# Kernel tuning notes

Hardware: AMD Instinct MI355X
Metric: run time of the kernel (lower is better)

## Reference

```python
import jax, jax.numpy as jnp
import numpy as np

B, L1, L2, H = 16, 1024, 1024, 768

def setup_inputs() -> dict:
    key = jax.random.key(0)
    k1, k2, k3, k4, k5, k6 = jax.random.split(key, 6)
    x1 = jax.random.normal(k1, (B, L1, H), dtype=jnp.float32)
    x2 = jax.random.normal(k2, (B, L2, H), dtype=jnp.float32)
    # True = padded position (masked out), matching torch masked_fill_ semantics
    x1_mask = jax.random.randint(k3, (B, L1), 0, 2) == 1
    x2_mask = jax.random.randint(k4, (B, L2), 0, 2) == 1
    # shared nn.Linear(H, H) used for both x and y projections
    W = jax.random.normal(k5, (H, H), dtype=jnp.float32) / np.sqrt(H)
    b = jax.random.normal(k6, (H,), dtype=jnp.float32) * 0.01
    return {"x1": x1, "x2": x2, "x1_mask": x1_mask, "x2_mask": x2_mask, "W": W, "b": b}

def reference(x1, x2, x1_mask, x2_mask, W, b):
    # SeqAttnMatch('relu_FC', normalize='sumY') with z = y = x2
    x_proj = jax.nn.relu(jnp.einsum('bid,hd->bih', x1, W) + b)   # [B,L1,H]
    y_proj = jax.nn.relu(jnp.einsum('bjd,hd->bjh', x2, W) + b)   # [B,L2,H]
    scores = jnp.einsum('bih,bjh->bij', x_proj, y_proj)          # [B,L1,L2]
    scores = jnp.where(x2_mask[:, None, :], -jnp.inf, scores)
    alpha = jax.nn.softmax(scores, axis=-1)                      # sum over len2
    att = jnp.einsum('bij,bjd->bid', alpha, x2)                  # [B,L1,H]
    # inter_att_concat = 'concat_dot_diff'
    return jnp.concatenate([x1, att, x1 * att, x1 - att], axis=2)  # [B,L1,4H]
```

## Files before the change

### kernel.cpp

```cpp
#include <hip/hip_runtime.h>


#define B_  16
#define L_  1024
#define H_  768
#define M1_ (B_ * L_)
#define MT_ (2 * M1_)

#define XB_  24576
#define WB_  576
#define TB_  3072

using f32x4  = __attribute__((ext_vector_type(4))) float;
using bf16x8 = __attribute__((ext_vector_type(8))) __bf16;
using u16x8  = __attribute__((ext_vector_type(8))) unsigned short;
using u16x4  = __attribute__((ext_vector_type(4))) unsigned short;

__device__ inline unsigned short f2b(float f) {
  unsigned u = __builtin_bit_cast(unsigned, f);
  u += 0x7FFFu + ((u >> 16) & 1u);
  return (unsigned short)(u >> 16);
}
__device__ inline float b2f(unsigned short u) {
  return __builtin_bit_cast(float, ((unsigned)u) << 16);
}

__device__ inline void gld16(const void* g, void* l) {
  __builtin_amdgcn_global_load_lds(
      (__attribute__((address_space(1))) void*)g,
      (__attribute__((address_space(3))) void*)l, 16, 0, 0);
}

__device__ inline bf16x8 ld_frag_sw(const unsigned short* lds, int row, int quad) {
  const int sl = quad ^ ((row >> 1) & 3);
  u16x8 v = *(const u16x8*)(lds + row * 32 + sl * 8);
  return __builtin_bit_cast(bf16x8, v);
}

#define MFMA(a, b, c) __builtin_amdgcn_mfma_f32_16x16x32_bf16((a), (b), (c), 0, 0, 0)

__device__ __forceinline__ void stage2(const unsigned short* __restrict__ src,
                                       unsigned short* ldsbase,
                                       int wv, int lq, int lsw,
                                       size_t row0, int k0) {
#pragma unroll
  for (int g = 0; g < 2; ++g) {
    const int rowl = wv * 32 + g * 16;
    gld16(src + (row0 + rowl + lq) * (size_t)H_ + k0 + lsw * 8,
          ldsbase + rowl * 32);
  }
}

__device__ __forceinline__ void gemm3_loop(
    const unsigned short* __restrict__ Agh, const unsigned short* __restrict__ Agl,
    const unsigned short* __restrict__ Bgh, const unsigned short* __restrict__ Bgl,
    size_t arow0, size_t brow0,
    unsigned short* SA, unsigned short* SB, f32x4 (&acc)[8][4])
{
  const int tid  = threadIdx.x;
  const int lane = tid & 63, wv = tid >> 6;
  const int wr = wv >> 2, wc = wv & 3;
  const int quad = lane >> 4, lx = lane & 15;
  const int lq  = lane >> 2;
  const int lsw = (lane & 3) ^ ((lane >> 3) & 3);
  constexpr int HB = 256 * 32;

  stage2(Agh, SA,      wv, lq, lsw, arow0, 0);
  stage2(Bgh, SB,      wv, lq, lsw, brow0, 0);
  stage2(Agl, SA + HB, wv, lq, lsw, arow0, 0);
  stage2(Bgl, SB + HB, wv, lq, lsw, brow0, 0);
  asm volatile("s_waitcnt vmcnt(4)" ::: "memory");
  __builtin_amdgcn_s_barrier();

  int c = 0;
  for (int t = 0; t < H_ / 32; ++t) {
    unsigned short* sAh = SA + c * (2 * HB);
    unsigned short* sAl = sAh + HB;
    unsigned short* sBh = SB + c * (2 * HB);
    unsigned short* sBl = sBh + HB;
    unsigned short* dA  = SA + (c ^ 1) * (2 * HB);
    unsigned short* dB  = SB + (c ^ 1) * (2 * HB);
    const int  k1   = t * 32 + 32;
    const bool more = (t < H_ / 32 - 1);

    bf16x8 fah[8], fbh[4];
#pragma unroll
    for (int i = 0; i < 8; ++i) fah[i] = ld_frag_sw(sAh, wr * 128 + i * 16 + lx, quad);
#pragma unroll
    for (int j = 0; j < 4; ++j) fbh[j] = ld_frag_sw(sBh, wc * 64 + j * 16 + lx, quad);
    if (more) {
      stage2(Agh, dA,      wv, lq, lsw, arow0, k1);
      stage2(Bgh, dB,      wv, lq, lsw, brow0, k1);
      stage2(Agl, dA + HB, wv, lq, lsw, arow0, k1);
      stage2(Bgl, dB + HB, wv, lq, lsw, brow0, k1);
    }
    __builtin_amdgcn_s_barrier();
    __builtin_amdgcn_s_setprio(1);
#pragma unroll
    for (int i = 0; i < 8; ++i)
#pragma unroll
      for (int j = 0; j < 4; ++j) acc[i][j] = MFMA(fah[i], fbh[j], acc[i][j]);
    __builtin_amdgcn_s_setprio(0);
    if (more) asm volatile("s_waitcnt vmcnt(8)" ::: "memory");
    else      asm volatile("s_waitcnt vmcnt(0)" ::: "memory");
    __builtin_amdgcn_s_barrier();

    bf16x8 fbl[4];
#pragma unroll
    for (int j = 0; j < 4; ++j) fbl[j] = ld_frag_sw(sBl, wc * 64 + j * 16 + lx, quad);
    __builtin_amdgcn_s_barrier();
    __builtin_amdgcn_s_setprio(1);
#pragma unroll
    for (int i = 0; i < 8; ++i)
#pragma unroll
      for (int j = 0; j < 4; ++j) acc[i][j] = MFMA(fah[i], fbl[j], acc[i][j]);
    __builtin_amdgcn_s_setprio(0);
    __builtin_amdgcn_s_barrier();

    bf16x8 fal[8];
#pragma unroll
    for (int i = 0; i < 8; ++i) fal[i] = ld_frag_sw(sAl, wr * 128 + i * 16 + lx, quad);
    __builtin_amdgcn_s_barrier();
    __builtin_amdgcn_s_setprio(1);
#pragma unroll
    for (int i = 0; i < 8; ++i)
#pragma unroll
      for (int j = 0; j < 4; ++j) acc[i][j] = MFMA(fal[i], fbh[j], acc[i][j]);
    __builtin_amdgcn_s_setprio(0);
    if (more) asm volatile("s_waitcnt vmcnt(4)" ::: "memory");
    __builtin_amdgcn_s_barrier();

    c ^= 1;
  }
}

__global__ __launch_bounds__(256) void k_split(
    const float* __restrict__ x1, const float* __restrict__ x2,
    const float* __restrict__ W,
    unsigned short* __restrict__ Xh, unsigned short* __restrict__ Xl,
    unsigned short* __restrict__ Wh, unsigned short* __restrict__ Wl,
    unsigned short* __restrict__ x2T)
{
  __shared__ unsigned short tile[64][72];
  const int tid = threadIdx.x;
  const int bx  = blockIdx.x;

  if (bx < XB_) {
    const size_t idx = (size_t)bx * 256 + tid;
    const int row = (int)(idx / 192);
    const int col = ((int)(idx % 192)) * 4;
    const float* src = (row < M1_) ? (x1 + (size_t)row * H_ + col)
                                   : (x2 + (size_t)(row - M1_) * H_ + col);
    f32x4 v = *(const f32x4*)src;
    u16x4 h, l;
#pragma unroll
    for (int q = 0; q < 4; ++q) { h[q] = f2b(v[q]); l[q] = f2b(v[q] - b2f(h[q])); }
    *(u16x4*)(Xh + idx * 4) = h;
    *(u16x4*)(Xl + idx * 4) = l;
  } else if (bx < XB_ + WB_) {
    const int idx = (bx - XB_) * 256 + tid;
    f32x4 v = *(const f32x4*)(W + (size_t)idx * 4);
    u16x4 h, l;
#pragma unroll
    for (int q = 0; q < 4; ++q) { h[q] = f2b(v[q]); l[q] = f2b(v[q] - b2f(h[q])); }
    *(u16x4*)(Wh + (size_t)idx * 4) = h;
    *(u16x4*)(Wl + (size_t)idx * 4) = l;
  } else {
    const int t  = bx - (XB_ + WB_);
    const int b  = t / 192;
    const int r  = t % 192;
    const int j0 = (r / 12) * 64;
    const int d0 = (r % 12) * 64;
#pragma unroll
    for (int p = 0; p < 4; ++p) {
      const int idx = tid + p * 256;
      const int jr  = idx >> 4;
      const int dc  = (idx & 15) * 4;
      f32x4 v = *(const f32x4*)(x2 + ((size_t)(b * L_ + j0 + jr)) * H_ + d0 + dc);
#pragma unroll
      for (int q = 0; q < 4; ++q) tile[jr][dc + q] = f2b(v[q]);
    }
    __syncthreads();
#pragma unroll
    for (int p = 0; p < 2; ++p) {
      const int idx = tid + p * 256;
      const int dr  = idx >> 3;
      const int jc  = (idx & 7) * 8;
      u16x8 o;
#pragma unroll
      for (int q = 0; q < 8; ++q) o[q] = tile[jc + q][dr];
      *(u16x8*)(x2T + ((size_t)(b * H_) + d0 + dr) * L_ + j0 + jc) = o;
    }
  }
}

__global__ __launch_bounds__(512, 2) void k_proj(
    const unsigned short* __restrict__ Xh, const unsigned short* __restrict__ Xl,
    const unsigned short* __restrict__ Wh, const unsigned short* __restrict__ Wl,
    const float* __restrict__ bias,
    unsigned short* __restrict__ Ph, unsigned short* __restrict__ Pl)
{
  __shared__ unsigned short SA[2 * 2 * 256 * 32];
  __shared__ unsigned short SB[2 * 2 * 256 * 32];

  const int tid  = threadIdx.x;
  const int lane = tid & 63, wv = tid >> 6;
  const int wr = wv >> 2, wc = wv & 3;
  const int quad = lane >> 4, lx = lane & 15;

  const int lin = blockIdx.x;
  const int s   = (lin & 7) * 48 + (lin >> 3);
  const int n0  = (s % 3) * 256;
  const int m0  = (s / 3) * 256;

  f32x4 acc[8][4] = {};
  gemm3_loop(Xh, Xl, Wh, Wl, (size_t)m0, (size_t)n0, SA, SB, acc);

#pragma unroll
  for (int j = 0; j < 4; ++j) {
    const int h = n0 + wc * 64 + j * 16 + lx;
    const float bv = bias[h];
#pragma unroll
    for (int i = 0; i < 8; ++i) {
      const int mrow = m0 + wr * 128 + i * 16 + quad * 4;
#pragma unroll
      for (int r = 0; r < 4; ++r) {
        float v = acc[i][j][r] + bv;
        v = v > 0.f ? v : 0.f;
        const unsigned short hh = f2b(v);
        const unsigned short ll = f2b(v - b2f(hh));
        const size_t off = (size_t)(mrow + r) * H_ + h;
        Ph[off] = hh;
        Pl[off] = ll;
      }
    }
  }
}

__global__ __launch_bounds__(512, 2) void k_scores(
    const unsigned short* __restrict__ Ph, const unsigned short* __restrict__ Pl,
    const int* __restrict__ x2_mask, float* __restrict__ scores)
{
  __shared__ unsigned short SA[2 * 2 * 256 * 32];
  __shared__ unsigned short SB[2 * 2 * 256 * 32];

  const int tid  = threadIdx.x;
  const int lane = tid & 63, wv = tid >> 6;
  const int wr = wv >> 2, wc = wv & 3;
  const int quad = lane >> 4, lx = lane & 15;

  const int lin = blockIdx.x;
  const int s   = (lin & 7) * 32 + (lin >> 3);
  const int j0  = (s & 3) * 256;
  const int i0  = ((s >> 2) & 3) * 256;
  const int b   = s >> 4;

  f32x4 acc[8][4] = {};
  gemm3_loop(Ph, Pl, Ph, Pl,
             (size_t)(b * L_ + i0), (size_t)(M1_ + b * L_ + j0), SA, SB, acc);

#pragma unroll
  for (int j = 0; j < 4; ++j) {
    const int jj = j0 + wc * 64 + j * 16 + lx;
    const int mv = x2_mask[b * L_ + jj];
#pragma unroll
    for (int i = 0; i < 8; ++i) {
      const int ib = i0 + wr * 128 + i * 16 + quad * 4;
#pragma unroll
      for (int r = 0; r < 4; ++r) {
        const float v = mv ? -1e30f : acc[i][j][r];
        scores[((size_t)(b * L_) + ib + r) * L_ + jj] = v;
      }
    }
  }
}

__global__ __launch_bounds__(256) void k_softmax(
    const float* __restrict__ scores, unsigned short* __restrict__ alphab)
{
  const size_t row = blockIdx.x;
  const float* p = scores + row * L_;
  const int tid = threadIdx.x;

  f32x4 v = *(const f32x4*)(p + tid * 4);
  float m = fmaxf(fmaxf(v[0], v[1]), fmaxf(v[2], v[3]));
#pragma unroll
  for (int off = 32; off > 0; off >>= 1) m = fmaxf(m, __shfl_down(m, off));

  __shared__ float rmax[4];
  __shared__ float rsum[4];
  const int wid = tid >> 6, lane = tid & 63;
  if (lane == 0) rmax[wid] = m;
  __syncthreads();
  m = fmaxf(fmaxf(rmax[0], rmax[1]), fmaxf(rmax[2], rmax[3]));

  f32x4 e;
#pragma unroll
  for (int q = 0; q < 4; ++q) e[q] = __expf(v[q] - m);
  float s = e[0] + e[1] + e[2] + e[3];
#pragma unroll
  for (int off = 32; off > 0; off >>= 1) s += __shfl_down(s, off);
  if (lane == 0) rsum[wid] = s;
  __syncthreads();
  s = rsum[0] + rsum[1] + rsum[2] + rsum[3];

  const float inv = 1.0f / s;
  u16x4 o;
#pragma unroll
  for (int q = 0; q < 4; ++q) o[q] = f2b(e[q] * inv);
  *(u16x4*)(alphab + row * L_ + tid * 4) = o;
}

__global__ __launch_bounds__(256) void k_att(
    const unsigned short* __restrict__ alphab, const unsigned short* __restrict__ x2T,
    float* __restrict__ att)
{
  __shared__ unsigned short Aa[128 * 32];
  __shared__ unsigned short Bt[128 * 32];

  const int tid  = threadIdx.x;
  const int lane = tid & 63, wv = tid >> 6;
  const int wr = wv >> 1, wc = wv & 1;
  const int quad = lane >> 4, lx = lane & 15;
  const int lr = lane >> 2, ls = lane & 3;
  const int lsw = ls ^ ((lr >> 1) & 3);

  const int lin = blockIdx.x;
  const int s   = (lin & 7) * 96 + (lin >> 3);
  const int d0  = (s % 6) * 128;
  const int i0  = ((s / 6) & 7) * 128;
  const int b   = s / 48;

  f32x4 acc[4][4] = {};

  for (int j0 = 0; j0 < L_; j0 += 32) {
    __syncthreads();
#pragma unroll
    for (int g = 0; g < 2; ++g) {
      const int rowl = wv * 32 + g * 16;
      const int row  = rowl + lr;
      const size_t ga = (size_t)(b * L_ + i0 + row) * L_ + j0 + lsw * 8;
      const size_t gb = ((size_t)(b * H_) + d0 + row) * L_ + j0 + lsw * 8;
      gld16(alphab + ga, &Aa[rowl * 32]);
      gld16(x2T + gb, &Bt[rowl * 32]);
    }
    __syncthreads();

    bf16x8 fa[4], fb[4];
#pragma unroll
    for (int t = 0; t < 4; ++t) {
      fa[t] = ld_frag_sw(Aa, wr * 64 + t * 16 + lx, quad);
      fb[t] = ld_frag_sw(Bt, wc * 64 + t * 16 + lx, quad);
    }
#pragma unroll
    for (int i = 0; i < 4; ++i)
#pragma unroll
      for (int j = 0; j < 4; ++j)
        acc[i][j] = MFMA(fa[i], fb[j], acc[i][j]);
  }

#pragma unroll
  for (int j = 0; j < 4; ++j) {
    const int dd = d0 + wc * 64 + j * 16 + lx;
#pragma unroll
    for (int i = 0; i < 4; ++i) {
      const int ib = i0 + wr * 64 + i * 16 + quad * 4;
#pragma unroll
      for (int r = 0; r < 4; ++r)
        att[((size_t)(b * L_) + ib + r) * H_ + dd] = acc[i][j][r];
    }
  }
}

__global__ __launch_bounds__(256) void k_concat(
    const float* __restrict__ x1, const float* __restrict__ att,
    float* __restrict__ out)
{
  const int gid = blockIdx.x * 256 + threadIdx.x;
  const int row = gid / 192;
  const int c   = (gid % 192) * 4;

  f32x4 xv = *(const f32x4*)(x1  + (size_t)row * H_ + c);
  f32x4 av = *(const f32x4*)(att + (size_t)row * H_ + c);
  f32x4 mv, sv;
#pragma unroll
  for (int q = 0; q < 4; ++q) { mv[q] = xv[q] * av[q]; sv[q] = xv[q] - av[q]; }

  float* ob = out + (size_t)row * (4 * H_) + c;
  *(f32x4*)(ob)          = xv;
  *(f32x4*)(ob + H_)     = av;
  *(f32x4*)(ob + 2 * H_) = mv;
  *(f32x4*)(ob + 3 * H_) = sv;
}

extern "C" void kernel_launch(void* const* d_in, const int* in_sizes, int n_in,
                              void* d_out, int out_size, void* d_ws, size_t ws_size,
                              hipStream_t stream) {
  const float* x1      = (const float*)d_in[0];
  const float* x2      = (const float*)d_in[1];
  const int*   x2_mask = (const int*)d_in[3];
  const float* W       = (const float*)d_in[4];
  const float* bias    = (const float*)d_in[5];
  float* out = (float*)d_out;

  char* o8 = (char*)d_out;
  unsigned short* Ph     = (unsigned short*)o8;
  unsigned short* Pl     = (unsigned short*)(o8 + 50331648);
  float*          scores = (float*)(o8 + 100663296);
  unsigned short* Xh     = (unsigned short*)(o8 + 100663296);
  unsigned short* Wh     = (unsigned short*)(o8 + 167772160);
  unsigned short* Wl     = (unsigned short*)(o8 + 168951808);
  unsigned short* x2T    = (unsigned short*)(o8 + 170131456);
  unsigned short* alphab = (unsigned short*)o8;
  unsigned short* Xl     = (unsigned short*)d_ws;
  float*          att    = (float*)d_ws;

  k_split  <<<dim3(XB_ + WB_ + TB_), 256, 0, stream>>>(x1, x2, W, Xh, Xl, Wh, Wl, x2T);
  k_proj   <<<dim3(384),   512, 0, stream>>>(Xh, Xl, Wh, Wl, bias, Ph, Pl);
  k_scores <<<dim3(256),   512, 0, stream>>>(Ph, Pl, x2_mask, scores);
  k_softmax<<<dim3(16384), 256, 0, stream>>>(scores, alphab);
  k_att    <<<dim3(768),   256, 0, stream>>>(alphab, x2T, att);
  k_concat <<<dim3(12288), 256, 0, stream>>>(x1, att, out);
}
```

Baseline: 644.0 us.

## Halve projection GEMM M-tile and stagger low-half loads across MFMA phases

The projection GEMM now uses 128x256 tiles instead of 256x256, which doubles the block count to 768 and halves the A-side shared memory. The shared GEMM loop is templated on the M-fragment count. Prefetches of the low-precision halves (Bl, Al) are moved later so they overlap the intermediate MFMA phases rather than all being issued at once, with vmcnt waits adjusted to match. This aims to improve CU occupancy and wave balance for the projection and to spread memory traffic through the loop. The cost is less operand reuse per block in the projection and more intricate wait-count bookkeeping.

```diff
diff --git a/kernel.cpp b/kernel.cpp
--- a/kernel.cpp
+++ b/kernel.cpp
@@ -39,95 +39,106 @@
 
 #define MFMA(a, b, c) __builtin_amdgcn_mfma_f32_16x16x32_bf16((a), (b), (c), 0, 0, 0)
 
-__device__ __forceinline__ void stage2(const unsigned short* __restrict__ src,
+template<int CH>
+__device__ __forceinline__ void stageH(const unsigned short* __restrict__ src,
                                        unsigned short* ldsbase,
                                        int wv, int lq, int lsw,
                                        size_t row0, int k0) {
 #pragma unroll
-  for (int g = 0; g < 2; ++g) {
-    const int rowl = wv * 32 + g * 16;
+  for (int g = 0; g < CH; ++g) {
+    const int rowl = wv * (CH * 16) + g * 16;
     gld16(src + (row0 + rowl + lq) * (size_t)H_ + k0 + lsw * 8,
           ldsbase + rowl * 32);
   }
 }
 
+template<int MI>
 __device__ __forceinline__ void gemm3_loop(
     const unsigned short* __restrict__ Agh, const unsigned short* __restrict__ Agl,
     const unsigned short* __restrict__ Bgh, const unsigned short* __restrict__ Bgl,
     size_t arow0, size_t brow0,
-    unsigned short* SA, unsigned short* SB, f32x4 (&acc)[8][4])
-{
+    unsigned short* SA, unsigned short* SB, f32x4 (&acc)[MI][4])
+{
+  constexpr int CA  = MI / 4;
+  constexpr int HBA = (MI * 32) * 32;
+  constexpr int HBB = 256 * 32;
+
   const int tid  = threadIdx.x;
   const int lane = tid & 63, wv = tid >> 6;
   const int wr = wv >> 2, wc = wv & 3;
   const int quad = lane >> 4, lx = lane & 15;
   const int lq  = lane >> 2;
   const int lsw = (lane & 3) ^ ((lane >> 3) & 3);
-  constexpr int HB = 256 * 32;
-
-  stage2(Agh, SA,      wv, lq, lsw, arow0, 0);
-  stage2(Bgh, SB,      wv, lq, lsw, brow0, 0);
-  stage2(Agl, SA + HB, wv, lq, lsw, arow0, 0);
-  stage2(Bgl, SB + HB, wv, lq, lsw, brow0, 0);
-  asm volatile("s_waitcnt vmcnt(4)" ::: "memory");
+
+  stageH<CA>(Agh, SA,       wv, lq, lsw, arow0, 0);
+  stageH<2 >(Bgh, SB,       wv, lq, lsw, brow0, 0);
+  stageH<2 >(Bgl, SB + HBB, wv, lq, lsw, brow0, 0);
+  stageH<CA>(Agl, SA + HBA, wv, lq, lsw, arow0, 0);
+  asm volatile("s_waitcnt vmcnt(%0)" :: "i"(CA + 2) : "memory");
   __builtin_amdgcn_s_barrier();
 
   int c = 0;
   for (int t = 0; t < H_ / 32; ++t) {
-    unsigned short* sAh = SA + c * (2 * HB);
-    unsigned short* sAl = sAh + HB;
-    unsigned short* sBh = SB + c * (2 * HB);
-    unsigned short* sBl = sBh + HB;
-    unsigned short* dA  = SA + (c ^ 1) * (2 * HB);
-    unsigned short* dB  = SB + (c ^ 1) * (2 * HB);
+    unsigned short* sAh = SA + c * (2 * HBA);
+    unsigned short* sAl = sAh + HBA;
+    unsigned short* sBh = SB + c * (2 * HBB);
+    unsigned short* sBl = sBh + HBB;
+    unsigned short* dA  = SA + (c ^ 1) * (2 * HBA);
+    unsigned short* dB  = SB + (c ^ 1) * (2 * HBB);
     const int  k1   = t * 32 + 32;
     const bool more = (t < H_ / 32 - 1);
 
-    bf16x8 fah[8], fbh[4];
-#pragma unroll
-    for (int i = 0; i < 8; ++i) fah[i] = ld_frag_sw(sAh, wr * 128 + i * 16 + lx, quad);
-#pragma unroll
-    for (int j = 0; j < 4; ++j) fbh[j] = ld_frag_sw(sBh, wc * 64 + j * 16 + lx, quad);
+    bf16x8 fah[MI], fbh[4];
+#pragma unroll
+    for (int i = 0; i < MI; ++i)
+      fah[i] = ld_frag_sw(sAh, wr * (MI * 16) + i * 16 + lx, quad);
+#pragma unroll
+    for (int j = 0; j < 4; ++j)
+      fbh[j] = ld_frag_sw(sBh, wc * 64 + j * 16 + lx, quad);
     if (more) {
-      stage2(Agh, dA,      wv, lq, lsw, arow0, k1);
-      stage2(Bgh, dB,      wv, lq, lsw, brow0, k1);
-      stage2(Agl, dA + HB, wv, lq, lsw, arow0, k1);
-      stage2(Bgl, dB + HB, wv, lq, lsw, brow0, k1);
+      stageH<CA>(Agh, dA, wv, lq, lsw, arow0, k1);
+      stageH<2 >(Bgh, dB, wv, lq, lsw, brow0, k1);
     }
     __builtin_amdgcn_s_barrier();
     __builtin_amdgcn_s_setprio(1);
 #pragma unroll
-    for (int i = 0; i < 8; ++i)
+    for (int i = 0; i < MI; ++i)
 #pragma unroll
       for (int j = 0; j < 4; ++j) acc[i][j] = MFMA(fah[i], fbh[j], acc[i][j]);
     __builtin_amdgcn_s_setprio(0);
-    if (more) asm volatile("s_waitcnt vmcnt(8)" ::: "memory");
-    else      asm volatile("s_waitcnt vmcnt(0)" ::: "memory");
+    if (more) asm volatile("s_waitcnt vmcnt(%0)" :: "i"(2 * CA + 2) : "memory");
+    else      asm volatile("s_waitcnt vmcnt(%0)" :: "i"(CA)         : "memory");
     __builtin_amdgcn_s_barrier();
 
     bf16x8 fbl[4];
 #pragma unroll
-    for (int j = 0; j < 4; ++j) fbl[j] = ld_frag_sw(sBl, wc * 64 + j * 16 + lx, quad);
+    for (int j = 0; j < 4; ++j)
+      fbl[j] = ld_frag_sw(sBl, wc * 64 + j * 16 + lx, quad);
+    if (more) stageH<2>(Bgl, dB + HBB, wv, lq, lsw, brow0, k1);
     __builtin_amdgcn_s_barrier();
     __builtin_amdgcn_s_setprio(1);
 #pragma unroll
-    for (int i = 0; i < 8; ++i)
+    for (int i = 0; i < MI; ++i)
 #pragma unroll
       for (int j = 0; j < 4; ++j) acc[i][j] = MFMA(fah[i], fbl[j], acc[i][j]);
     __builtin_amdgcn_s_setprio(0);
-    __builtin_amdgcn_s_barrier();
-
-    bf16x8 fal[8];
-#pragma unroll
-    for (int i = 0; i < 8; ++i) fal[i] = ld_frag_sw(sAl, wr * 128 + i * 16 + lx, quad);
+    if (more) asm volatile("s_waitcnt vmcnt(%0)" :: "i"(CA + 4) : "memory");
+    else      asm volatile("s_waitcnt vmcnt(0)" ::: "memory");
+    __builtin_amdgcn_s_barrier();
+
+    bf16x8 fal[MI];
+#pragma unroll
+    for (int i = 0; i < MI; ++i)
+      fal[i] = ld_frag_sw(sAl, wr * (MI * 16) + i * 16 + lx, quad);
+    if (more) stageH<CA>(Agl, dA + HBA, wv, lq, lsw, arow0, k1);
     __builtin_amdgcn_s_barrier();
     __builtin_amdgcn_s_setprio(1);
 #pragma unroll
-    for (int i = 0; i < 8; ++i)
+    for (int i = 0; i < MI; ++i)
 #pragma unroll
       for (int j = 0; j < 4; ++j) acc[i][j] = MFMA(fal[i], fbh[j], acc[i][j]);
     __builtin_amdgcn_s_setprio(0);
-    if (more) asm volatile("s_waitcnt vmcnt(4)" ::: "memory");
+    if (more) asm volatile("s_waitcnt vmcnt(%0)" :: "i"(CA + 2) : "memory");
     __builtin_amdgcn_s_barrier();
 
     c ^= 1;
@@ -200,7 +211,7 @@
     const float* __restrict__ bias,
     unsigned short* __restrict__ Ph, unsigned short* __restrict__ Pl)
 {
-  __shared__ unsigned short SA[2 * 2 * 256 * 32];
+  __shared__ unsigned short SA[2 * 2 * 128 * 32];
   __shared__ unsigned short SB[2 * 2 * 256 * 32];
 
   const int tid  = threadIdx.x;
@@ -209,20 +220,20 @@
   const int quad = lane >> 4, lx = lane & 15;
 
   const int lin = blockIdx.x;
-  const int s   = (lin & 7) * 48 + (lin >> 3);
+  const int s   = (lin & 7) * 96 + (lin >> 3);
   const int n0  = (s % 3) * 256;
-  const int m0  = (s / 3) * 256;
-
-  f32x4 acc[8][4] = {};
-  gemm3_loop(Xh, Xl, Wh, Wl, (size_t)m0, (size_t)n0, SA, SB, acc);
+  const int m0  = (s / 3) * 128;
+
+  f32x4 acc[4][4] = {};
+  gemm3_loop<4>(Xh, Xl, Wh, Wl, (size_t)m0, (size_t)n0, SA, SB, acc);
 
 #pragma unroll
   for (int j = 0; j < 4; ++j) {
     const int h = n0 + wc * 64 + j * 16 + lx;
     const float bv = bias[h];
 #pragma unroll
-    for (int i = 0; i < 8; ++i) {
-      const int mrow = m0 + wr * 128 + i * 16 + quad * 4;
+    for (int i = 0; i < 4; ++i) {
+      const int mrow = m0 + wr * 64 + i * 16 + quad * 4;
 #pragma unroll
       for (int r = 0; r < 4; ++r) {
         float v = acc[i][j][r] + bv;
@@ -256,8 +267,8 @@
   const int b   = s >> 4;
 
   f32x4 acc[8][4] = {};
-  gemm3_loop(Ph, Pl, Ph, Pl,
-             (size_t)(b * L_ + i0), (size_t)(M1_ + b * L_ + j0), SA, SB, acc);
+  gemm3_loop<8>(Ph, Pl, Ph, Pl,
+                (size_t)(b * L_ + i0), (size_t)(M1_ + b * L_ + j0), SA, SB, acc);
 
 #pragma unroll
   for (int j = 0; j < 4; ++j) {
@@ -416,7 +427,7 @@
   float*          att    = (float*)d_ws;
 
   k_split  <<<dim3(XB_ + WB_ + TB_), 256, 0, stream>>>(x1, x2, W, Xh, Xl, Wh, Wl, x2T);
-  k_proj   <<<dim3(384),   512, 0, stream>>>(Xh, Xl, Wh, Wl, bias, Ph, Pl);
+  k_proj   <<<dim3(768),   512, 0, stream>>>(Xh, Xl, Wh, Wl, bias, Ph, Pl);
   k_scores <<<dim3(256),   512, 0, stream>>>(Ph, Pl, x2_mask, scores);
   k_softmax<<<dim3(16384), 256, 0, stream>>>(scores, alphab);
   k_att    <<<dim3(768),   256, 0, stream>>>(alphab, x2T, att);
```

Result: faster. 588.5 us (-8.6%).
